# Optimization experiments

Measured on AMD Instinct MI355X. Metric: run time of the kernel, lower is better.

## Reference

```python
import jax, jax.numpy as jnp
import numpy as np

D_MODEL = 768
N_HEAD = 12


def setup_inputs() -> dict:
    key = jax.random.key(0)
    ks = jax.random.split(key, 5)
    B, S, D = 2, 4096, D_MODEL
    scale = 0.02
    return {
        "x": jax.random.normal(ks[0], (B, S, D), dtype=jnp.float32),
        "W_in": jax.random.normal(ks[1], (D, 3 * D), dtype=jnp.float32) * scale,
        "b_in": jax.random.normal(ks[2], (3 * D,), dtype=jnp.float32) * scale,
        "W_out": jax.random.normal(ks[3], (D, D), dtype=jnp.float32) * scale,
        "b_out": jax.random.normal(ks[4], (D,), dtype=jnp.float32) * scale,
    }


def reference(x, W_in, b_in, W_out, b_out):
    B, S, D = x.shape
    H = N_HEAD
    d_head = D // H
    qkv = x @ W_in + b_in                      # [B,S,3D]
    q, k, v = jnp.split(qkv, 3, axis=-1)
    # [B,H,S,d]
    q = q.reshape(B, S, H, d_head).transpose(0, 2, 1, 3)
    k = k.reshape(B, S, H, d_head).transpose(0, 2, 1, 3)
    v = v.reshape(B, S, H, d_head).transpose(0, 2, 1, 3)
    att = jnp.einsum("bhqd,bhkd->bhqk", q, k) * (1.0 / jnp.sqrt(jnp.float32(d_head)))
    causal = jnp.tril(jnp.ones((S, S), dtype=bool))
    att = jnp.where(causal[None, None], att, jnp.float32(-jnp.inf))
    att = jax.nn.softmax(att, axis=-1)
    y = jnp.einsum("bhqk,bhkd->bhqd", att, v)  # [B,H,S,d]
    y = y.transpose(0, 2, 1, 3).reshape(B, S, D)
    return y @ W_out + b_out
```

## Files before the change

kernel.cpp:

```cpp
#include <hip/hip_runtime.h>
#include <hip/hip_bf16.h>


#define D_MODEL 768
#define SEQ 4096
#define NB 2
#define NHEAD 12
#define LDQK 1536

typedef __attribute__((ext_vector_type(8))) short short8;
typedef __attribute__((ext_vector_type(4))) float floatx4;

#define SM_C 0.18033688011112042f

#if __has_builtin(__builtin_amdgcn_exp2f)
#define EXP2(x) __builtin_amdgcn_exp2f(x)
#else
#define EXP2(x) __expf((x) * 0.6931471805599453f)
#endif

__device__ inline short fb(float f) {
    union { __hip_bfloat16 h; short s; } cv;
    cv.h = __float2bfloat16(f);
    return cv.s;
}
__device__ inline unsigned pk2(float a, float b) {
    float2 f; f.x = a; f.y = b;
    union { __hip_bfloat162 h; unsigned u; } cv;
    cv.h = __float22bfloat162_rn(f);
    return cv.u;
}
__device__ inline void gload16(const void* g, void* l) {
    __builtin_amdgcn_global_load_lds(
        (const __attribute__((address_space(1))) unsigned int*)g,
        (__attribute__((address_space(3))) unsigned int*)l, 16, 0, 0);
}

__global__ __launch_bounds__(256) void convert_bf16(const float* __restrict__ src,
                                                    short* __restrict__ dst, size_t n) {
    size_t i = ((size_t)blockIdx.x * 256 + threadIdx.x) * 8;
    if (i >= n) return;
    float4 f0 = *(const float4*)(src + i);
    float4 f1 = *(const float4*)(src + i + 4);
    uint4 u = {pk2(f0.x, f0.y), pk2(f0.z, f0.w), pk2(f1.x, f1.y), pk2(f1.z, f1.w)};
    *(uint4*)(dst + i) = u;
}

__global__ __launch_bounds__(256) void transpose_bf16(const float* __restrict__ W,
                                                      short* __restrict__ Wt,
                                                      int K, int N) {
    __shared__ short t[32][33];
    const int n0 = blockIdx.x * 32, k0 = blockIdx.y * 32;
    const int tx = threadIdx.x, ty = threadIdx.y;
#pragma unroll
    for (int j = 0; j < 4; ++j)
        t[ty + j * 8][tx] = fb(W[(size_t)(k0 + ty + j * 8) * N + n0 + tx]);
    __syncthreads();
#pragma unroll
    for (int j = 0; j < 4; ++j)
        Wt[(size_t)(n0 + ty + j * 8) * K + k0 + tx] = t[tx][ty + j * 8];
}

__global__ __launch_bounds__(256) void gemm_qkv128(const short* __restrict__ A,
                                                   const short* __restrict__ Bt,
                                                   const float* __restrict__ bias,
                                                   short* __restrict__ qkw,
                                                   short* __restrict__ vtw) {
    const int K = D_MODEL;
    __shared__ short As[128][32];
    __shared__ short Bs[128][32];
    const int tid = threadIdx.x, lane = tid & 63, w = tid >> 6;
    const int wr = w >> 1, wc = w & 1;
    const int lo = lane & 15, hi = lane >> 4;
    const int m0 = blockIdx.y * 128, n0 = blockIdx.x * 128;
    const int lr = lane >> 2, lc = (lane & 3) * 8;

    floatx4 acc[4][4] = {};
    const short* Ag = A  + (size_t)(m0 + w * 16 + lr) * K + lc;
    const short* Bg = Bt + (size_t)(n0 + w * 16 + lr) * K + lc;

    for (int k0 = 0; k0 < K; k0 += 32) {
        __syncthreads();
        gload16(Ag + k0,                  &As[w * 16][0]);
        gload16(Ag + k0 + (size_t)64 * K, &As[64 + w * 16][0]);
        gload16(Bg + k0,                  &Bs[w * 16][0]);
        gload16(Bg + k0 + (size_t)64 * K, &Bs[64 + w * 16][0]);
        __syncthreads();
        short8 a[4], bf[4];
#pragma unroll
        for (int m = 0; m < 4; ++m) a[m] = *(const short8*)&As[wr * 64 + m * 16 + lo][hi * 8];
#pragma unroll
        for (int n = 0; n < 4; ++n) bf[n] = *(const short8*)&Bs[wc * 64 + n * 16 + lo][hi * 8];
#pragma unroll
        for (int m = 0; m < 4; ++m)
#pragma unroll
            for (int n = 0; n < 4; ++n)
                acc[m][n] = __builtin_amdgcn_mfma_f32_16x16x32_bf16(a[m], bf[n], acc[m][n], 0, 0, 0);
    }

#pragma unroll
    for (int m = 0; m < 4; ++m)
#pragma unroll
        for (int n = 0; n < 4; ++n) {
            int col  = n0 + wc * 64 + n * 16 + lo;
            int row0 = m0 + wr * 64 + m * 16 + hi * 4;
            float bv = bias[col];
            if (col < LDQK) {
#pragma unroll
                for (int r = 0; r < 4; ++r)
                    qkw[(size_t)(row0 + r) * LDQK + col] = fb(acc[m][n][r] + bv);
            } else {
                int vcol = col - LDQK;
                int hh = vcol >> 6, dh = vcol & 63;
                int bb = row0 >> 12, s = row0 & 4095;
                uint2 u = {pk2(acc[m][n][0] + bv, acc[m][n][1] + bv),
                           pk2(acc[m][n][2] + bv, acc[m][n][3] + bv)};
                *(uint2*)&vtw[(((size_t)bb * NHEAD + hh) * 64 + dh) * SEQ + s] = u;
            }
        }
}

__global__ __launch_bounds__(256) void gemm_out128(const short* __restrict__ A,
                                                   const short* __restrict__ Bt,
                                                   const float* __restrict__ bias,
                                                   float* __restrict__ C) {
    const int K = D_MODEL, N = D_MODEL;
    __shared__ short As[128][32];
    __shared__ short Bs[128][32];
    const int tid = threadIdx.x, lane = tid & 63, w = tid >> 6;
    const int wr = w >> 1, wc = w & 1;
    const int lo = lane & 15, hi = lane >> 4;
    const int m0 = blockIdx.y * 128, n0 = blockIdx.x * 128;
    const int lr = lane >> 2, lc = (lane & 3) * 8;

    floatx4 acc[4][4] = {};
    const short* Ag = A  + (size_t)(m0 + w * 16 + lr) * K + lc;
    const short* Bg = Bt + (size_t)(n0 + w * 16 + lr) * K + lc;

    for (int k0 = 0; k0 < K; k0 += 32) {
        __syncthreads();
        gload16(Ag + k0,                  &As[w * 16][0]);
        gload16(Ag + k0 + (size_t)64 * K, &As[64 + w * 16][0]);
        gload16(Bg + k0,                  &Bs[w * 16][0]);
        gload16(Bg + k0 + (size_t)64 * K, &Bs[64 + w * 16][0]);
        __syncthreads();
        short8 a[4], bf[4];
#pragma unroll
        for (int m = 0; m < 4; ++m) a[m] = *(const short8*)&As[wr * 64 + m * 16 + lo][hi * 8];
#pragma unroll
        for (int n = 0; n < 4; ++n) bf[n] = *(const short8*)&Bs[wc * 64 + n * 16 + lo][hi * 8];
#pragma unroll
        for (int m = 0; m < 4; ++m)
#pragma unroll
            for (int n = 0; n < 4; ++n)
                acc[m][n] = __builtin_amdgcn_mfma_f32_16x16x32_bf16(a[m], bf[n], acc[m][n], 0, 0, 0);
    }

#pragma unroll
    for (int m = 0; m < 4; ++m)
#pragma unroll
        for (int n = 0; n < 4; ++n) {
            int col  = n0 + wc * 64 + n * 16 + lo;
            int row0 = m0 + wr * 64 + m * 16 + hi * 4;
            float bv = bias[col];
#pragma unroll
            for (int r = 0; r < 4; ++r)
                C[(size_t)(row0 + r) * N + col] = acc[m][n][r] + bv;
        }
}

__global__ __launch_bounds__(256) void attn_k(const short* __restrict__ qk,
                                              const short* __restrict__ vt,
                                              short* __restrict__ y) {
    const int L = blockIdx.x;
    const int xcd = L & 7, slot = L >> 3;
    const int gh = slot >> 5, ip = slot & 31;
    const int g = gh * 8 + xcd;
    const int b = g / NHEAD, h = g % NHEAD;

    const int tid = threadIdx.x, lane = tid & 63, w = tid >> 6;
    const int lo = lane & 15, hi = lane >> 4;

    __shared__ alignas(16) short Ks[64 * 64];
    __shared__ alignas(16) short Vs[64 * 64];
    __shared__ alignas(16) short Ps[4 * 16 * 64];

    const short* qbase = qk + (size_t)b * SEQ * LDQK;
    const short* kbase = qbase + D_MODEL;
    const short* vbase = vt + ((size_t)b * NHEAD + h) * 64 * SEQ;

    const int skey = tid >> 2, sdc = tid & 3;
    const int sdim = tid >> 2, skg = tid & 3;

    short* kcommit0 = &Ks[skey * 64 + (((sdc * 2)    ) ^ (skey & 7)) * 8];
    short* kcommit1 = &Ks[skey * 64 + (((sdc * 2) + 1) ^ (skey & 7)) * 8];
    short* vcommit0 = &Vs[sdim * 64 + (((skg * 2)    ) ^ (sdim & 7)) * 8];
    short* vcommit1 = &Vs[sdim * 64 + (((skg * 2) + 1) ^ (sdim & 7)) * 8];
    unsigned* pwbase = (unsigned*)&Ps[w * 1024];

    for (int t = 0; t < 2; ++t) {
        const int qt = t ? ip : 63 - ip;
        const int q0 = qt * 64;

        short8 qf[2];
        {
            const short* qrow = qbase + (size_t)(q0 + w * 16 + lo) * LDQK + h * 64;
            qf[0] = *(const short8*)(qrow + hi * 8);
            qf[1] = *(const short8*)(qrow + 32 + hi * 8);
        }

        floatx4 o[4] = {};
        float lrun = 0.0f;
        float sc4[4];

        const short* kptr = kbase + (size_t)skey * LDQK + h * 64 + sdc * 16;
        const short* vptr = vbase + (size_t)sdim * SEQ + skg * 16;
        short8 kpre[2], vpre[2];
        kpre[0] = *(const short8*)kptr;
        kpre[1] = *(const short8*)(kptr + 8);
        vpre[0] = *(const short8*)vptr;
        vpre[1] = *(const short8*)(vptr + 8);

        auto tile_body = [&](bool diag) {
            floatx4 sT[4];
            __builtin_amdgcn_s_setprio(1);
#pragma unroll
            for (int c = 0; c < 4; ++c) {
                floatx4 acc = {};
#pragma unroll
                for (int kc = 0; kc < 2; ++kc) {
                    short8 kf = *(const short8*)&Ks[(c * 16 + lo) * 64 + ((kc * 4 + hi) ^ (lo & 7)) * 8];
                    acc = __builtin_amdgcn_mfma_f32_16x16x32_bf16(kf, qf[kc], acc, 0, 0, 0);
                }
                sT[c] = acc;
            }
            __builtin_amdgcn_s_setprio(0);

            const int qin = w * 16 + lo;
            if (diag) {
#pragma unroll
                for (int c = 0; c < 4; ++c)
#pragma unroll
                    for (int r = 0; r < 4; ++r)
                        if ((c * 16 + hi * 4 + r) > qin) sT[c][r] = -1e30f;
            }

            float p[4][4];
            float rs = 0.0f;
#pragma unroll
            for (int c = 0; c < 4; ++c)
#pragma unroll
                for (int r = 0; r < 4; ++r) {
                    float e = EXP2(sT[c][r] * SM_C);
                    p[c][r] = e;
                    rs += e;
                }
            lrun += rs;

#pragma unroll
            for (int c = 0; c < 4; ++c) {
                uint2 word = {pk2(p[c][0], p[c][1]), pk2(p[c][2], p[c][3])};
                *(uint2*)(pwbase + ((lo * 64 + (((c * 4 + hi) ^ (lo & 14)) * 4)) >> 1)) = word;
            }
            asm volatile("s_waitcnt lgkmcnt(0)" ::: "memory");

            __builtin_amdgcn_s_setprio(1);
#pragma unroll
            for (int kc = 0; kc < 2; ++kc) {
                short8 af = *(const short8*)&Ps[w * 1024 + lo * 64 + ((kc * 8 + hi * 2) ^ (lo & 14)) * 4];
#pragma unroll
                for (int dc = 0; dc < 4; ++dc) {
                    short8 vf = *(const short8*)&Vs[(dc * 16 + lo) * 64 + ((kc * 4 + hi) ^ (lo & 7)) * 8];
                    o[dc] = __builtin_amdgcn_mfma_f32_16x16x32_bf16(af, vf, o[dc], 0, 0, 0);
                }
            }
            __builtin_amdgcn_s_setprio(0);
        };

        for (int kb = 0; kb < qt; ++kb) {
            __syncthreads();
            *(short8*)kcommit0 = kpre[0];
            *(short8*)kcommit1 = kpre[1];
            *(short8*)vcommit0 = vpre[0];
            *(short8*)vcommit1 = vpre[1];
            __syncthreads();
            kptr += (size_t)64 * LDQK;
            vptr += 64;
            kpre[0] = *(const short8*)kptr;
            kpre[1] = *(const short8*)(kptr + 8);
            vpre[0] = *(const short8*)vptr;
            vpre[1] = *(const short8*)(vptr + 8);
            tile_body(false);
        }
        __syncthreads();
        *(short8*)kcommit0 = kpre[0];
        *(short8*)kcommit1 = kpre[1];
        *(short8*)vcommit0 = vpre[0];
        *(short8*)vcommit1 = vpre[1];
        __syncthreads();
        tile_body(true);

        lrun += __shfl_xor(lrun, 16, 64);
        lrun += __shfl_xor(lrun, 32, 64);
#pragma unroll
        for (int r = 0; r < 4; ++r) sc4[r] = __shfl(lrun, hi * 4 + r, 16);
#pragma unroll
        for (int r = 0; r < 4; ++r) {
            float inv = 1.0f / sc4[r];
            int row = q0 + w * 16 + hi * 4 + r;
            short* dst = y + ((size_t)b * SEQ + row) * D_MODEL + h * 64;
#pragma unroll
            for (int dc = 0; dc < 4; ++dc) dst[dc * 16 + lo] = fb(o[dc][r] * inv);
        }
    }
}

extern "C" void kernel_launch(void* const* d_in, const int* in_sizes, int n_in,
                              void* d_out, int out_size, void* d_ws, size_t ws_size,
                              hipStream_t stream) {
    (void)in_sizes; (void)n_in; (void)out_size; (void)ws_size;
    const float* x     = (const float*)d_in[0];
    const float* W_in  = (const float*)d_in[1];
    const float* b_in  = (const float*)d_in[2];
    const float* W_out = (const float*)d_in[3];
    const float* b_out = (const float*)d_in[4];
    float* out = (float*)d_out;

    const int M = NB * SEQ;
    char* p = (char*)d_ws;
    short* xbf   = (short*)p; p += (size_t)M * D_MODEL * 2;
    short* wtin  = (short*)p; p += (size_t)3 * D_MODEL * D_MODEL * 2;
    short* wtout = (short*)p; p += (size_t)D_MODEL * D_MODEL * 2;
    short* qkw   = (short*)p; p += (size_t)M * LDQK * 2;
    short* vtw   = (short*)p; p += (size_t)NB * NHEAD * 64 * SEQ * 2;
    short* yw    = (short*)p;

    convert_bf16<<<dim3((unsigned)((size_t)M * D_MODEL / 8 / 256)), 256, 0, stream>>>(
        x, xbf, (size_t)M * D_MODEL);
    transpose_bf16<<<dim3(3 * D_MODEL / 32, D_MODEL / 32), dim3(32, 8), 0, stream>>>(
        W_in, wtin, D_MODEL, 3 * D_MODEL);
    transpose_bf16<<<dim3(D_MODEL / 32, D_MODEL / 32), dim3(32, 8), 0, stream>>>(
        W_out, wtout, D_MODEL, D_MODEL);
    gemm_qkv128<<<dim3(3 * D_MODEL / 128, M / 128), 256, 0, stream>>>(
        xbf, wtin, b_in, qkw, vtw);
    attn_k<<<dim3(NB * NHEAD * (SEQ / 128)), 256, 0, stream>>>(qkw, vtw, yw);
    gemm_out128<<<dim3(D_MODEL / 128, M / 128), 256, 0, stream>>>(yw, wtout, b_out, out);
}
```

Baseline: 188.3 us.

## Split attention work across wave pairs with 32x32 MFMA and folded softmax scale

Rewrites the causal attention kernel so that two wave-pairs each process a balanced share of key blocks for the paired short and long query tiles in a single 33-iteration loop. The long tile's partial output and row sums are merged through shared memory at the end, instead of processing the two tiles one after another. The kernel now uses 32x32x16 MFMA and keeps P in registers via v_permlane32_swap rather than a shared-memory round trip. The softmax scale is folded into Q inside the QKV GEMM epilogue. This adds a double K/V buffer, larger accumulators with register-pressure risk under launch_bounds(256,4), and a final cross-pair reduction.

```diff
diff --git a/kernel.cpp b/kernel.cpp
--- a/kernel.cpp
+++ b/kernel.cpp
@@ -10,6 +10,7 @@
 
 typedef __attribute__((ext_vector_type(8))) short short8;
 typedef __attribute__((ext_vector_type(4))) float floatx4;
+typedef __attribute__((ext_vector_type(16))) float floatx16;
 
 #define SM_C 0.18033688011112042f
 
@@ -107,8 +108,11 @@
             float bv = bias[col];
             if (col < LDQK) {
 #pragma unroll
-                for (int r = 0; r < 4; ++r)
-                    qkw[(size_t)(row0 + r) * LDQK + col] = fb(acc[m][n][r] + bv);
+                for (int r = 0; r < 4; ++r) {
+                    float v = acc[m][n][r] + bv;
+                    if (col < D_MODEL) v *= SM_C;
+                    qkw[(size_t)(row0 + r) * LDQK + col] = fb(v);
+                }
             } else {
                 int vcol = col - LDQK;
                 int hh = vcol >> 6, dh = vcol & 63;
@@ -169,149 +173,194 @@
         }
 }
 
-__global__ __launch_bounds__(256) void attn_k(const short* __restrict__ qk,
-                                              const short* __restrict__ vt,
-                                              short* __restrict__ y) {
+__global__ __launch_bounds__(256, 4) void attn_k(const short* __restrict__ qk,
+                                                 const short* __restrict__ vt,
+                                                 short* __restrict__ y) {
     const int L = blockIdx.x;
     const int xcd = L & 7, slot = L >> 3;
-    const int gh = slot >> 5, ip = slot & 31;
-    const int g = gh * 8 + xcd;
+    const int ghead = slot >> 5, ip = slot & 31;
+    const int g = ghead * 8 + xcd;
     const int b = g / NHEAD, h = g % NHEAD;
 
     const int tid = threadIdx.x, lane = tid & 63, w = tid >> 6;
-    const int lo = lane & 15, hi = lane >> 4;
-
-    __shared__ alignas(16) short Ks[64 * 64];
-    __shared__ alignas(16) short Vs[64 * 64];
-    __shared__ alignas(16) short Ps[4 * 16 * 64];
+    const int q32 = lane & 31, hh = lane >> 5;
+    const int pairB = w >> 1;
+    const int wrow = (w & 1) * 32;
+
+    __shared__ alignas(16) short KVs[2][2][64 * 64];
+    __shared__ float Lcmb[128];
 
     const short* qbase = qk + (size_t)b * SEQ * LDQK;
     const short* kbase = qbase + D_MODEL;
     const short* vbase = vt + ((size_t)b * NHEAD + h) * 64 * SEQ;
 
-    const int skey = tid >> 2, sdc = tid & 3;
-    const int sdim = tid >> 2, skg = tid & 3;
-
-    short* kcommit0 = &Ks[skey * 64 + (((sdc * 2)    ) ^ (skey & 7)) * 8];
-    short* kcommit1 = &Ks[skey * 64 + (((sdc * 2) + 1) ^ (skey & 7)) * 8];
-    short* vcommit0 = &Vs[sdim * 64 + (((skg * 2)    ) ^ (sdim & 7)) * 8];
-    short* vcommit1 = &Vs[sdim * 64 + (((skg * 2) + 1) ^ (sdim & 7)) * 8];
-    unsigned* pwbase = (unsigned*)&Ps[w * 1024];
-
-    for (int t = 0; t < 2; ++t) {
-        const int qt = t ? ip : 63 - ip;
-        const int q0 = qt * 64;
-
-        short8 qf[2];
+    short* Kb = KVs[pairB][0];
+    short* Vb = KVs[pairB][1];
+
+    const int lt = tid & 127;
+    const int srow = lt >> 1, shalf = lt & 1;
+    int cof[4];
+#pragma unroll
+    for (int jj = 0; jj < 4; ++jj)
+        cof[jj] = srow * 64 + ((shalf * 4 + jj) ^ (srow & 7)) * 8;
+
+    const int qt_hi = 63 - ip, qt_lo = ip;
+    int tq0 = (pairB ? qt_lo : qt_hi) * 64;
+
+    short8 qf[4];
+    {
+        const short* qr = qbase + (size_t)(tq0 + wrow + q32) * LDQK + h * 64 + hh * 8;
+        qf[0] = *(const short8*)(qr);
+        qf[1] = *(const short8*)(qr + 16);
+        qf[2] = *(const short8*)(qr + 32);
+        qf[3] = *(const short8*)(qr + 48);
+    }
+
+    floatx16 O0 = {}, O1 = {};
+    float lsum = 0.0f;
+
+    short8 kpre[4], vpre[4];
+    {
+        const short* kg = kbase + (size_t)srow * LDQK + h * 64 + shalf * 32;
+        const short* vg = vbase + (size_t)srow * SEQ + shalf * 32;
+#pragma unroll
+        for (int jj = 0; jj < 4; ++jj) {
+            kpre[jj] = *(const short8*)(kg + jj * 8);
+            vpre[jj] = *(const short8*)(vg + jj * 8);
+        }
+    }
+    int curblk = 0;
+
+    auto store_out = [&](float ltot) {
+        float inv = 1.0f / ltot;
+#pragma unroll
+        for (int r = 0; r < 16; ++r) {
+            int qrow = (r & 3) + 8 * (r >> 2) + 4 * hh;
+            float iv = __shfl(inv, qrow, 64);
+            short* d = y + ((size_t)b * SEQ + tq0 + wrow + qrow) * D_MODEL + h * 64;
+            d[q32]      = fb(O0[r] * iv);
+            d[32 + q32] = fb(O1[r] * iv);
+        }
+    };
+
+    for (int j = 0; j <= 32; ++j) {
+        __syncthreads();
+        if (curblk >= 0) {
+#pragma unroll
+            for (int jj = 0; jj < 4; ++jj) {
+                *(short8*)&Kb[cof[jj]] = kpre[jj];
+                *(short8*)&Vb[cof[jj]] = vpre[jj];
+            }
+        }
+        __syncthreads();
+
+        int nxt;
         {
-            const short* qrow = qbase + (size_t)(q0 + w * 16 + lo) * LDQK + h * 64;
-            qf[0] = *(const short8*)(qrow + hi * 8);
-            qf[1] = *(const short8*)(qrow + 32 + hi * 8);
-        }
-
-        floatx4 o[4] = {};
-        float lrun = 0.0f;
-        float sc4[4];
-
-        const short* kptr = kbase + (size_t)skey * LDQK + h * 64 + sdc * 16;
-        const short* vptr = vbase + (size_t)sdim * SEQ + skg * 16;
-        short8 kpre[2], vpre[2];
-        kpre[0] = *(const short8*)kptr;
-        kpre[1] = *(const short8*)(kptr + 8);
-        vpre[0] = *(const short8*)vptr;
-        vpre[1] = *(const short8*)(vptr + 8);
-
-        auto tile_body = [&](bool diag) {
-            floatx4 sT[4];
-            __builtin_amdgcn_s_setprio(1);
-#pragma unroll
-            for (int c = 0; c < 4; ++c) {
-                floatx4 acc = {};
-#pragma unroll
-                for (int kc = 0; kc < 2; ++kc) {
-                    short8 kf = *(const short8*)&Ks[(c * 16 + lo) * 64 + ((kc * 4 + hi) ^ (lo & 7)) * 8];
-                    acc = __builtin_amdgcn_mfma_f32_16x16x32_bf16(kf, qf[kc], acc, 0, 0, 0);
-                }
-                sT[c] = acc;
+            int jn = j + 1;
+            if (!pairB) nxt = (jn <= 32) ? jn : -1;
+            else        nxt = (jn <= ip) ? jn : (jn <= 31 ? 32 + (jn - ip) : -1);
+        }
+        if (nxt >= 0) {
+            const short* kg = kbase + (size_t)(nxt * 64 + srow) * LDQK + h * 64 + shalf * 32;
+            const short* vg = vbase + (size_t)srow * SEQ + nxt * 64 + shalf * 32;
+#pragma unroll
+            for (int jj = 0; jj < 4; ++jj) {
+                kpre[jj] = *(const short8*)(kg + jj * 8);
+                vpre[jj] = *(const short8*)(vg + jj * 8);
             }
-            __builtin_amdgcn_s_setprio(0);
-
-            const int qin = w * 16 + lo;
-            if (diag) {
-#pragma unroll
-                for (int c = 0; c < 4; ++c)
-#pragma unroll
-                    for (int r = 0; r < 4; ++r)
-                        if ((c * 16 + hi * 4 + r) > qin) sT[c][r] = -1e30f;
+        }
+
+        if (pairB && j == ip + 1) {
+            float ltot = lsum + __shfl_xor(lsum, 32, 64);
+            store_out(ltot);
+#pragma unroll
+            for (int r = 0; r < 16; ++r) { O0[r] = 0.0f; O1[r] = 0.0f; }
+            lsum = 0.0f;
+            tq0 = qt_hi * 64;
+            const short* qr = qbase + (size_t)(tq0 + wrow + q32) * LDQK + h * 64 + hh * 8;
+            qf[0] = *(const short8*)(qr);
+            qf[1] = *(const short8*)(qr + 16);
+            qf[2] = *(const short8*)(qr + 32);
+            qf[3] = *(const short8*)(qr + 48);
+        }
+
+        if (curblk >= 0) {
+            const int myqt = (pairB && j <= ip) ? qt_lo : qt_hi;
+            const bool diag = (curblk == myqt);
+
+#pragma unroll
+            for (int kb2 = 0; kb2 < 2; ++kb2) {
+                floatx16 S = {};
+                __builtin_amdgcn_s_setprio(1);
+#pragma unroll
+                for (int kc = 0; kc < 4; ++kc) {
+                    short8 kf = *(const short8*)&Kb[(kb2 * 32 + q32) * 64 + ((kc * 2 + hh) ^ (q32 & 7)) * 8];
+                    S = __builtin_amdgcn_mfma_f32_32x32x16_bf16(kf, qf[kc], S, 0, 0, 0);
+                }
+                __builtin_amdgcn_s_setprio(0);
+
+                if (diag) {
+                    int qg = tq0 + wrow + q32;
+                    int kb_base = curblk * 64 + kb2 * 32 + 4 * hh;
+#pragma unroll
+                    for (int r = 0; r < 16; ++r) {
+                        int kgl = kb_base + (r & 3) + 8 * (r >> 2);
+                        if (kgl > qg) S[r] = -1e30f;
+                    }
+                }
+
+                unsigned wA[4], wB[4];
+#pragma unroll
+                for (int g4 = 0; g4 < 4; ++g4) {
+                    float p0 = EXP2(S[4 * g4 + 0]), p1 = EXP2(S[4 * g4 + 1]);
+                    float p2 = EXP2(S[4 * g4 + 2]), p3 = EXP2(S[4 * g4 + 3]);
+                    lsum += (p0 + p1) + (p2 + p3);
+                    wA[g4] = pk2(p0, p1);
+                    wB[g4] = pk2(p2, p3);
+                }
+#pragma unroll
+                for (int c16 = 0; c16 < 2; ++c16) {
+                    unsigned xa = wA[2 * c16], ya = wA[2 * c16 + 1];
+                    unsigned xb = wB[2 * c16], yb = wB[2 * c16 + 1];
+                    asm("v_permlane32_swap_b32 %0, %1" : "+v"(xa), "+v"(ya));
+                    asm("v_permlane32_swap_b32 %0, %1" : "+v"(xb), "+v"(yb));
+                    union { unsigned u[4]; short8 s; } pa;
+                    pa.u[0] = xa; pa.u[1] = xb; pa.u[2] = ya; pa.u[3] = yb;
+                    const int kc = kb2 * 2 + c16;
+                    short8 vf0 = *(const short8*)&Vb[q32 * 64 + ((kc * 2 + hh) ^ (q32 & 7)) * 8];
+                    short8 vf1 = *(const short8*)&Vb[(32 + q32) * 64 + ((kc * 2 + hh) ^ (q32 & 7)) * 8];
+                    __builtin_amdgcn_s_setprio(1);
+                    O0 = __builtin_amdgcn_mfma_f32_32x32x16_bf16(pa.s, vf0, O0, 0, 0, 0);
+                    O1 = __builtin_amdgcn_mfma_f32_32x32x16_bf16(pa.s, vf1, O1, 0, 0, 0);
+                    __builtin_amdgcn_s_setprio(0);
+                }
             }
-
-            float p[4][4];
-            float rs = 0.0f;
-#pragma unroll
-            for (int c = 0; c < 4; ++c)
-#pragma unroll
-                for (int r = 0; r < 4; ++r) {
-                    float e = EXP2(sT[c][r] * SM_C);
-                    p[c][r] = e;
-                    rs += e;
-                }
-            lrun += rs;
-
-#pragma unroll
-            for (int c = 0; c < 4; ++c) {
-                uint2 word = {pk2(p[c][0], p[c][1]), pk2(p[c][2], p[c][3])};
-                *(uint2*)(pwbase + ((lo * 64 + (((c * 4 + hi) ^ (lo & 14)) * 4)) >> 1)) = word;
-            }
-            asm volatile("s_waitcnt lgkmcnt(0)" ::: "memory");
-
-            __builtin_amdgcn_s_setprio(1);
-#pragma unroll
-            for (int kc = 0; kc < 2; ++kc) {
-                short8 af = *(const short8*)&Ps[w * 1024 + lo * 64 + ((kc * 8 + hi * 2) ^ (lo & 14)) * 4];
-#pragma unroll
-                for (int dc = 0; dc < 4; ++dc) {
-                    short8 vf = *(const short8*)&Vs[(dc * 16 + lo) * 64 + ((kc * 4 + hi) ^ (lo & 7)) * 8];
-                    o[dc] = __builtin_amdgcn_mfma_f32_16x16x32_bf16(af, vf, o[dc], 0, 0, 0);
-                }
-            }
-            __builtin_amdgcn_s_setprio(0);
-        };
-
-        for (int kb = 0; kb < qt; ++kb) {
-            __syncthreads();
-            *(short8*)kcommit0 = kpre[0];
-            *(short8*)kcommit1 = kpre[1];
-            *(short8*)vcommit0 = vpre[0];
-            *(short8*)vcommit1 = vpre[1];
-            __syncthreads();
-            kptr += (size_t)64 * LDQK;
-            vptr += 64;
-            kpre[0] = *(const short8*)kptr;
-            kpre[1] = *(const short8*)(kptr + 8);
-            vpre[0] = *(const short8*)vptr;
-            vpre[1] = *(const short8*)(vptr + 8);
-            tile_body(false);
-        }
-        __syncthreads();
-        *(short8*)kcommit0 = kpre[0];
-        *(short8*)kcommit1 = kpre[1];
-        *(short8*)vcommit0 = vpre[0];
-        *(short8*)vcommit1 = vpre[1];
-        __syncthreads();
-        tile_body(true);
-
-        lrun += __shfl_xor(lrun, 16, 64);
-        lrun += __shfl_xor(lrun, 32, 64);
-#pragma unroll
-        for (int r = 0; r < 4; ++r) sc4[r] = __shfl(lrun, hi * 4 + r, 16);
-#pragma unroll
-        for (int r = 0; r < 4; ++r) {
-            float inv = 1.0f / sc4[r];
-            int row = q0 + w * 16 + hi * 4 + r;
-            short* dst = y + ((size_t)b * SEQ + row) * D_MODEL + h * 64;
-#pragma unroll
-            for (int dc = 0; dc < 4; ++dc) dst[dc * 16 + lo] = fb(o[dc][r] * inv);
-        }
+        }
+        curblk = nxt;
+    }
+
+    if (pairB) {
+        float* cO = (float*)&KVs[1][0][0];
+        const int lane2 = (w & 1) * 64 + lane;
+#pragma unroll
+        for (int r = 0; r < 16; ++r) {
+            cO[r * 128 + lane2]        = O0[r];
+            cO[(16 + r) * 128 + lane2] = O1[r];
+        }
+        Lcmb[lane2] = lsum;
+    }
+    __syncthreads();
+    if (!pairB) {
+        const float* cO = (const float*)&KVs[1][0][0];
+        const int lane2 = (w & 1) * 64 + lane;
+#pragma unroll
+        for (int r = 0; r < 16; ++r) {
+            O0[r] += cO[r * 128 + lane2];
+            O1[r] += cO[(16 + r) * 128 + lane2];
+        }
+        lsum += Lcmb[lane2];
+        float ltot = lsum + __shfl_xor(lsum, 32, 64);
+        store_out(ltot);
     }
 }
 
```

New measurement: 249.7 us. 32.6% more time.
